# Performance work log

Hardware: AMD Instinct MI355X
Metric: run time of the kernel (lower is better)

The kernel has to match this reference:

```python
import jax, jax.numpy as jnp
import numpy as np

N_NODES = 50000


def setup_inputs() -> dict:
    key = jax.random.key(0)
    k_x, k_e, k_w1, k_w2 = jax.random.split(key, 4)
    in_c, hid, out_c = 256, 128, 64
    x = jax.random.normal(k_x, (N_NODES, in_c), dtype=jnp.float32)
    edge_index = jax.random.randint(k_e, (2, 800000), 0, N_NODES, dtype=jnp.int64)
    # Glorot-ish scaled weights (faithful to GCNConv default init scale)
    W1 = jax.random.normal(k_w1, (in_c, hid), dtype=jnp.float32) * (1.0 / np.sqrt(in_c))
    b1 = jnp.zeros((hid,), dtype=jnp.float32)
    W2 = jax.random.normal(k_w2, (hid, out_c), dtype=jnp.float32) * (1.0 / np.sqrt(hid))
    b2 = jnp.zeros((out_c,), dtype=jnp.float32)
    return {"x": x, "edge_index": edge_index, "W1": W1, "b1": b1, "W2": W2, "b2": b2}


def _gcn_norm(edge_index, n_nodes):
    # Add self loops, compute symmetric normalization D^-1/2 A D^-1/2.
    loop = jnp.arange(n_nodes, dtype=edge_index.dtype)
    src = jnp.concatenate([edge_index[0], loop])
    dst = jnp.concatenate([edge_index[1], loop])
    deg = jax.ops.segment_sum(jnp.ones_like(dst, dtype=jnp.float32), dst,
                              num_segments=n_nodes)
    dis = jnp.where(deg > 0, jax.lax.rsqrt(deg), 0.0)  # deg_inv_sqrt
    norm = dis[src] * dis[dst]  # [E + N]
    return src, dst, norm


def _gcn_conv(x, W, b, src, dst, norm, n_nodes):
    h = x @ W                                  # [N, F_out] dense transform first
    msgs = h[src] * norm[:, None]              # edge-wise gather + scale
    agg = jax.ops.segment_sum(msgs, dst, num_segments=n_nodes)  # scatter-add
    return agg + b


def reference(x, edge_index, W1, b1, W2, b2):
    n = x.shape[0]
    src, dst, norm = _gcn_norm(edge_index, n)  # cached=True: same norm both layers
    h = _gcn_conv(x, W1, b1, src, dst, norm, n)
    h = jax.nn.relu(h)
    # Dropout is identity in eval mode (deterministic reference)
    return _gcn_conv(h, W2, b2, src, dst, norm, n)
```

## Files before the change

kernel.cpp:

```cpp
#include <hip/hip_runtime.h>


#define IN_C 256
#define HID 128
#define OUTC 64
#define NBLK 128

typedef __attribute__((ext_vector_type(8))) short short8;
typedef __attribute__((ext_vector_type(4))) float f32x4;

__device__ __forceinline__ void gload_lds16(const void* src, void* dst) {
    __builtin_amdgcn_global_load_lds(
        (const __attribute__((address_space(1))) unsigned int*)src,
        (__attribute__((address_space(3))) unsigned int*)dst, 16, 0, 0);
}

__device__ __forceinline__ void bf16split(float f, ushort& h, ushort& l) {
    unsigned u = __float_as_uint(f);
    h = (ushort)(u >> 16);
    float hf = __uint_as_float(u & 0xFFFF0000u);
    unsigned v = __float_as_uint(f - hf);
    l = (ushort)((v + 0x7FFF + ((v >> 16) & 1)) >> 16);
}

__device__ __forceinline__ void cvt8(float4 f0, float4 f1, short8& hi8, short8& lo8) {
    float ff[8];
    *(float4*)&ff[0] = f0; *(float4*)&ff[4] = f1;
    unsigned* hp = (unsigned*)&hi8;
    unsigned* lp = (unsigned*)&lo8;
    #pragma unroll
    for (int i = 0; i < 4; ++i) {
        unsigned u0 = __float_as_uint(ff[2 * i]), u1 = __float_as_uint(ff[2 * i + 1]);
        unsigned hf0 = u0 & 0xFFFF0000u, hf1 = u1 & 0xFFFF0000u;
        hp[i] = (u0 >> 16) | hf1;
        float r0 = ff[2 * i]     - __uint_as_float(hf0);
        float r1 = ff[2 * i + 1] - __uint_as_float(hf1);
        lp[i] = (__float_as_uint(r0) >> 16) | (__float_as_uint(r1) & 0xFFFF0000u);
    }
}

__device__ __forceinline__ ushort f2bf(float f) {
    unsigned u = __float_as_uint(f);
    return (ushort)((u + 0x7FFF + ((u >> 16) & 1)) >> 16);
}
__device__ __forceinline__ float bf2f(ushort u) {
    return __uint_as_float((unsigned)u << 16);
}

__device__ __forceinline__ int edge_at(const void* ei, long long idx, int is32) {
    return is32 ? ((const int*)ei)[idx] : (int)((const long long*)ei)[idx];
}

__global__ void detect_kernel(const unsigned long long* ei, int* flag) {
    if (threadIdx.x == 0 && blockIdx.x == 0) {
        int is32 = 0;
        for (int i = 0; i < 64; ++i)
            if (ei[i] >> 32) { is32 = 1; break; }
        *flag = is32;
    }
}

__global__ __launch_bounds__(256) void wtrans_kernel(const float* __restrict__ W1,
                                                     const float* __restrict__ W2,
                                                     ushort* __restrict__ wf1,
                                                     ushort* __restrict__ wf2) {
    int id = blockIdx.x * 256 + threadIdx.x;
    if (id < 8192) {
        int lane = id & 63, r = id >> 6;
        int pl = r & 1, nt = (r >> 1) & 7, kidx = r >> 4;
        int n = nt * 16 + (lane & 15);
        int kb = kidx * 32 + (lane >> 4) * 8;
        ushort v[8];
        #pragma unroll
        for (int j = 0; j < 8; ++j) {
            ushort h, l; bf16split(W1[(kb + j) * HID + n], h, l);
            v[j] = pl ? l : h;
        }
        *(short8*)&wf1[(size_t)id * 8] = *(short8*)v;
    } else if (id < 10240) {
        int id2 = id - 8192;
        int lane = id2 & 63, r = id2 >> 6;
        int pl = r & 1, nt = (r >> 1) & 3, kidx = r >> 3;
        int n = nt * 16 + (lane & 15);
        int kb = kidx * 32 + (lane >> 4) * 8;
        ushort v[8];
        #pragma unroll
        for (int j = 0; j < 8; ++j) {
            ushort h, l; bf16split(W2[(kb + j) * OUTC + n], h, l);
            v[j] = pl ? l : h;
        }
        *(short8*)&wf2[(size_t)id2 * 8] = *(short8*)v;
    }
}

__global__ __launch_bounds__(256) void bin_count(const void* ei, const int* __restrict__ flag,
                                                 int* __restrict__ blkcnt, int E, int nb) {
    __shared__ int h[256];
    int t = threadIdx.x;
    h[t] = 0;
    __syncthreads();
    int is32 = *flag;
    int chunk = (E + gridDim.x - 1) / gridDim.x;
    long long s0 = (long long)blockIdx.x * chunk;
    long long s1 = s0 + chunk; if (s1 > E) s1 = E;
    for (long long e = s0 + t; e < s1; e += 256) {
        int d = edge_at(ei, (long long)E + e, is32);
        atomicAdd(&h[d >> 8], 1);
    }
    __syncthreads();
    if (t < nb) blkcnt[t * NBLK + blockIdx.x] = h[t];
}

__global__ __launch_bounds__(256) void bin_scan(int* __restrict__ blkcnt,
                                                int* __restrict__ bbase, int nb) {
    __shared__ int sh[256];
    int t = threadIdx.x;
    int tot = 0;
    if (t < nb) {
        int4* p = (int4*)&blkcnt[t * NBLK];
        int run = 0;
        for (int i = 0; i < NBLK / 4; ++i) {
            int4 v = p[i]; int4 o;
            o.x = run; run += v.x; o.y = run; run += v.y;
            o.z = run; run += v.z; o.w = run; run += v.w;
            p[i] = o;
        }
        tot = run;
    }
    sh[t] = tot;
    __syncthreads();
    for (int d = 1; d < 256; d <<= 1) {
        int add = (t >= d) ? sh[t - d] : 0;
        __syncthreads();
        sh[t] += add;
        __syncthreads();
    }
    if (t < nb) {
        bbase[t] = sh[t] - tot;
        if (t == nb - 1) bbase[nb] = sh[t];
    }
}

__global__ __launch_bounds__(256) void bin_scatter(const void* ei, const int* __restrict__ flag,
                                                   const int* __restrict__ blkcnt,
                                                   const int* __restrict__ bbase,
                                                   unsigned* __restrict__ coarse, int E, int nb) {
    __shared__ int cur[256];
    int t = threadIdx.x;
    if (t < nb) cur[t] = bbase[t] + blkcnt[t * NBLK + blockIdx.x];
    __syncthreads();
    int is32 = *flag;
    int chunk = (E + gridDim.x - 1) / gridDim.x;
    long long s0 = (long long)blockIdx.x * chunk;
    long long s1 = s0 + chunk; if (s1 > E) s1 = E;
    for (long long e = s0 + t; e < s1; e += 256) {
        int s = edge_at(ei, e, is32);
        int d = edge_at(ei, (long long)E + e, is32);
        int p = atomicAdd(&cur[d >> 8], 1);
        coarse[p] = (unsigned)s | ((unsigned)(d & 255) << 17);
    }
}

__global__ __launch_bounds__(256) void fine_kernel(const unsigned* __restrict__ coarse,
                                                   const int* __restrict__ bbase,
                                                   int* __restrict__ row_ptr,
                                                   float* __restrict__ dis,
                                                   int* __restrict__ epk, int N, int nb) {
    __shared__ int h[256], cur[256], sh[256];
    int b = blockIdx.x, t = threadIdx.x;
    int nb0 = b << 8;
    int e0b = bbase[b], e1b = bbase[b + 1];
    h[t] = 0;
    __syncthreads();
    for (int e = e0b + t; e < e1b; e += 256)
        atomicAdd(&h[(coarse[e] >> 17) & 0xFF], 1);
    __syncthreads();
    int cnt = h[t];
    sh[t] = cnt;
    __syncthreads();
    for (int d = 1; d < 256; d <<= 1) {
        int add = (t >= d) ? sh[t - d] : 0;
        __syncthreads();
        sh[t] += add;
        __syncthreads();
    }
    int excl = sh[t] - cnt;
    int node = nb0 + t;
    if (node < N) {
        row_ptr[node] = e0b + excl;
        dis[node] = rsqrtf((float)cnt + 1.0f);
        if (node == N - 1) row_ptr[N] = e0b + sh[t];
    }
    cur[t] = e0b + excl;
    __syncthreads();
    for (int e = e0b + t; e < e1b; e += 256) {
        unsigned r = coarse[e];
        int p = atomicAdd(&cur[(r >> 17) & 0xFF], 1);
        epk[p] = (int)(r & 0x1FFFF);
    }
}

__global__ void zsent_kernel(ushort* a, ushort* b, ushort* c) {
    int t = threadIdx.x;
    if (t < 64) { a[t] = 0; b[t] = 0; c[t] = 0; }
}

__global__ __launch_bounds__(256) void gemm1_mfma(const float* __restrict__ X,
                                                  const ushort* __restrict__ wf1,
                                                  const float* __restrict__ dis,
                                                  ushort* __restrict__ HB, int N) {
    __shared__ float xs[64 * 64];
    int t = threadIdx.x;
    int lane = t & 63, w = t >> 6;
    int m_off = (w >> 1) * 32, n_off = (w & 1) * 64;
    long long row0 = (long long)blockIdx.x * 64;
    size_t sstride = (size_t)(N + 1) * 64;
    f32x4 acc[2][4] = {};
    for (int k0i = 0; k0i < 4; ++k0i) {
        __syncthreads();
        #pragma unroll
        for (int i = 0; i < 4; ++i) {
            int lrow = w * 16 + i * 4 + (lane >> 4);
            long long gr = row0 + lrow; if (gr >= N) gr = N - 1;
            int gchunk = (lane & 15) ^ (lrow & 7);
            gload_lds16(X + gr * IN_C + k0i * 64 + gchunk * 4,
                        xs + (w * 16 + i * 4) * 64);
        }
        __syncthreads();
        #pragma unroll
        for (int kk = 0; kk < 2; ++kk) {
            int kidx = k0i * 2 + kk;
            short8 ah[2], al[2], bh[4], bl[4];
            #pragma unroll
            for (int ni = 0; ni < 4; ++ni) {
                int nt = (n_off >> 4) + ni;
                const ushort* bp = wf1 + (size_t)(kidx * 16 + nt * 2) * 512 + lane * 8;
                bh[ni] = *(const short8*)bp;
                bl[ni] = *(const short8*)(bp + 512);
            }
            #pragma unroll
            for (int mi = 0; mi < 2; ++mi) {
                int r = m_off + mi * 16 + (lane & 15);
                int s = r & 7;
                int c0 = kk * 8 + (lane >> 4) * 2;
                float4 f0 = *(float4*)((char*)xs + r * 256 + ((c0 ^ s) * 16));
                float4 f1 = *(float4*)((char*)xs + r * 256 + (((c0 + 1) ^ s) * 16));
                cvt8(f0, f1, ah[mi], al[mi]);
            }
            #pragma unroll
            for (int mi = 0; mi < 2; ++mi)
                #pragma unroll
                for (int ni = 0; ni < 4; ++ni) {
                    acc[mi][ni] = __builtin_amdgcn_mfma_f32_16x16x32_bf16(ah[mi], bh[ni], acc[mi][ni], 0, 0, 0);
                    acc[mi][ni] = __builtin_amdgcn_mfma_f32_16x16x32_bf16(ah[mi], bl[ni], acc[mi][ni], 0, 0, 0);
                    acc[mi][ni] = __builtin_amdgcn_mfma_f32_16x16x32_bf16(al[mi], bh[ni], acc[mi][ni], 0, 0, 0);
                }
        }
    }
    int cr = (lane >> 4) * 4, cc = lane & 15;
    #pragma unroll
    for (int mi = 0; mi < 2; ++mi)
        #pragma unroll
        for (int j = 0; j < 4; ++j) {
            long long gr = row0 + m_off + mi * 16 + cr + j;
            if (gr < N) {
                float dv = dis[gr];
                #pragma unroll
                for (int ni = 0; ni < 4; ++ni) {
                    int col = n_off + ni * 16 + cc;
                    HB[(size_t)(col >> 6) * sstride + gr * 64 + (col & 63)] =
                        f2bf(acc[mi][ni][j] * dv);
                }
            }
        }
}

__global__ __launch_bounds__(256) void gemm2_mfma(const ushort* __restrict__ Ah,
                                                  const ushort* __restrict__ Al,
                                                  const ushort* __restrict__ wf2,
                                                  const float* __restrict__ dis,
                                                  ushort* __restrict__ HB, int N) {
    __shared__ ushort ash[64 * 64], asl[64 * 64];
    int t = threadIdx.x;
    int lane = t & 63, w = t >> 6;
    int m_off = (w >> 1) * 32, n_off = (w & 1) * 32;
    long long row0 = (long long)blockIdx.x * 64;
    f32x4 acc[2][2] = {};
    for (int k0i = 0; k0i < 2; ++k0i) {
        __syncthreads();
        #pragma unroll
        for (int i = 0; i < 2; ++i) {
            int rbase = w * 16 + i * 8;
            long long gr = row0 + rbase + (lane >> 3);
            size_t so = (size_t)gr * 128 + k0i * 64 + (lane & 7) * 8;
            gload_lds16(Ah + so, ash + rbase * 64);
            gload_lds16(Al + so, asl + rbase * 64);
        }
        __syncthreads();
        #pragma unroll
        for (int kk = 0; kk < 2; ++kk) {
            int kidx = k0i * 2 + kk;
            short8 ah[2], al[2], bh[2], bl[2];
            #pragma unroll
            for (int ni = 0; ni < 2; ++ni) {
                int nt = (n_off >> 4) + ni;
                const ushort* bp = wf2 + (size_t)(kidx * 8 + nt * 2) * 512 + lane * 8;
                bh[ni] = *(const short8*)bp;
                bl[ni] = *(const short8*)(bp + 512);
            }
            #pragma unroll
            for (int mi = 0; mi < 2; ++mi) {
                int r = m_off + mi * 16 + (lane & 15);
                int pos = (kk * 4 + (lane >> 4)) ^ (r & 7);
                ah[mi] = *(short8*)((char*)ash + r * 128 + pos * 16);
                al[mi] = *(short8*)((char*)asl + r * 128 + pos * 16);
            }
            #pragma unroll
            for (int mi = 0; mi < 2; ++mi)
                #pragma unroll
                for (int ni = 0; ni < 2; ++ni) {
                    acc[mi][ni] = __builtin_amdgcn_mfma_f32_16x16x32_bf16(ah[mi], bh[ni], acc[mi][ni], 0, 0, 0);
                    acc[mi][ni] = __builtin_amdgcn_mfma_f32_16x16x32_bf16(ah[mi], bl[ni], acc[mi][ni], 0, 0, 0);
                    acc[mi][ni] = __builtin_amdgcn_mfma_f32_16x16x32_bf16(al[mi], bh[ni], acc[mi][ni], 0, 0, 0);
                }
        }
    }
    int cr = (lane >> 4) * 4, cc = lane & 15;
    #pragma unroll
    for (int mi = 0; mi < 2; ++mi)
        #pragma unroll
        for (int j = 0; j < 4; ++j) {
            long long gr = row0 + m_off + mi * 16 + cr + j;
            if (gr < N) {
                float dv = dis[gr];
                #pragma unroll
                for (int ni = 0; ni < 2; ++ni)
                    HB[gr * OUTC + n_off + ni * 16 + cc] = f2bf(acc[mi][ni][j] * dv);
            }
        }
}

template <int MODE>
__global__ __launch_bounds__(256) void seg_agg_v6(const ushort* __restrict__ Hsl,
                                                  const float* __restrict__ dis,
                                                  const int* __restrict__ row_ptr,
                                                  const int* __restrict__ epk,
                                                  const float* __restrict__ bias,
                                                  float* __restrict__ outF,
                                                  ushort* __restrict__ outH,
                                                  ushort* __restrict__ outL,
                                                  int N, int sl) {
    int lane = threadIdx.x & 63;
    int node = (int)(((long long)blockIdx.x * blockDim.x + threadIdx.x) >> 6);
    if (node >= N) return;
    const ushort* hl = Hsl + lane;
    float acc = bf2f(hl[node * 64]);
    int e0 = row_ptr[node], e1 = row_ptr[node + 1];
    for (int base = e0; base < e1; base += 64) {
        int cnt = min(64, e1 - base);
        int rec = epk[min(base + lane, e1 - 1)];
        for (int u0 = 0; u0 < cnt; u0 += 16) {
            float hv[16];
            #pragma unroll
            for (int u = 0; u < 16; ++u) {
                int s = (u0 + u < cnt) ? __builtin_amdgcn_readlane(rec, u0 + u) : N;
                hv[u] = bf2f(hl[s * 64]);
            }
            #pragma unroll
            for (int u = 0; u < 16; ++u)
                acc += hv[u];
        }
    }
    float r = dis[node] * acc;
    if constexpr (MODE == 0) {
        float a2 = fmaxf(r + bias[sl * 64 + lane], 0.f);
        unsigned u = __float_as_uint(a2);
        ushort h = (ushort)(u >> 16);
        float rr = a2 - __uint_as_float(u & 0xFFFF0000u);
        ushort l = (ushort)(__float_as_uint(rr) >> 16);
        int col = sl * 64 + ((((lane >> 3) ^ (node & 7))) << 3) + (lane & 7);
        outH[(size_t)node * 128 + col] = h;
        outL[(size_t)node * 128 + col] = l;
    } else {
        outF[(size_t)node * 64 + lane] = r + bias[lane];
    }
}

extern "C" void kernel_launch(void* const* d_in, const int* in_sizes, int n_in,
                              void* d_out, int out_size, void* d_ws, size_t ws_size,
                              hipStream_t stream) {
    const float* x  = (const float*)d_in[0];
    const void*  ei = d_in[1];
    const float* W1 = (const float*)d_in[2];
    const float* b1 = (const float*)d_in[3];
    const float* W2 = (const float*)d_in[4];
    const float* b2 = (const float*)d_in[5];
    float* out = (float*)d_out;
    int N = in_sizes[0] / IN_C;
    int E = in_sizes[1] / 2;
    int nb = (N + 255) >> 8;
    int nblk64 = (N + 63) / 64;
    int N_pad = nblk64 * 64;

    char* ws = (char*)d_ws;
    size_t off = 0;
    auto alloc = [&](size_t bytes) {
        void* p = ws + off;
        off += ((bytes + 255) / 256) * 256;
        return p;
    };
    int*      flag    = (int*)alloc(4);
    int*      blkcnt  = (int*)alloc((size_t)nb * NBLK * 4);
    int*      bbase   = (int*)alloc(((size_t)nb + 1) * 4);
    int*      row_ptr = (int*)alloc(((size_t)N + 1) * 4);
    float*    dis     = (float*)alloc((size_t)N * 4);
    unsigned* coarse  = (unsigned*)alloc((size_t)E * 4);
    int*      epk     = (int*)alloc((size_t)E * 4);
    ushort*   wf1     = (ushort*)alloc(131072);
    ushort*   wf2     = (ushort*)alloc(32768);
    size_t sstride    = (size_t)(N + 1) * 64;
    ushort*   H1b     = (ushort*)alloc(2 * sstride * 2);
    ushort*   Ah      = (ushort*)alloc((size_t)N_pad * 128 * 2);
    ushort*   Al      = (ushort*)alloc((size_t)N_pad * 128 * 2);
    ushort*   H2b     = (ushort*)alloc(sstride * 2);

    detect_kernel<<<1, 64, 0, stream>>>((const unsigned long long*)ei, flag);
    wtrans_kernel<<<40, 256, 0, stream>>>(W1, W2, wf1, wf2);
    bin_count<<<NBLK, 256, 0, stream>>>(ei, flag, blkcnt, E, nb);
    bin_scan<<<1, 256, 0, stream>>>(blkcnt, bbase, nb);
    bin_scatter<<<NBLK, 256, 0, stream>>>(ei, flag, blkcnt, bbase, coarse, E, nb);
    fine_kernel<<<nb, 256, 0, stream>>>(coarse, bbase, row_ptr, dis, epk, N, nb);
    zsent_kernel<<<1, 64, 0, stream>>>(H1b + (size_t)N * 64,
                                       H1b + sstride + (size_t)N * 64,
                                       H2b + (size_t)N * 64);
    gemm1_mfma<<<nblk64, 256, 0, stream>>>(x, wf1, dis, H1b, N);

    int agg_blocks = (int)(((long long)N * 64 + 255) / 256);
    seg_agg_v6<0><<<agg_blocks, 256, 0, stream>>>(H1b,           dis, row_ptr, epk,
                                                  b1, nullptr, Ah, Al, N, 0);
    seg_agg_v6<0><<<agg_blocks, 256, 0, stream>>>(H1b + sstride, dis, row_ptr, epk,
                                                  b1, nullptr, Ah, Al, N, 1);
    gemm2_mfma<<<nblk64, 256, 0, stream>>>(Ah, Al, wf2, dis, H2b, N);
    seg_agg_v6<1><<<agg_blocks, 256, 0, stream>>>(H2b, dis, row_ptr, epk,
                                                  b2, out, nullptr, nullptr, N, 0);
}
```

Measured before the change: 160.2 us.

## Merge layer-1 aggregation launches, sort neighbors by source half, widen binning grid

Raises the number of binning blocks from 128 to 512 so the edge count and scatter pass is spread over more CUs. Within each destination node's neighbour list, the fine sort now groups sources into a lower and an upper half of the node range, which aims to improve gather locality in the L2/MALL. The two layer-1 aggregation launches are merged into one launch that covers both feature slices, removing a launch and its tail. The extra half-key doubles the LDS histogram and adds a compare per edge, and the per-block binning counts grow with the larger grid.

```diff
diff --git a/kernel.cpp b/kernel.cpp
--- a/kernel.cpp
+++ b/kernel.cpp
@@ -4,7 +4,7 @@
 #define IN_C 256
 #define HID 128
 #define OUTC 64
-#define NBLK 128
+#define NBLK 512
 
 typedef __attribute__((ext_vector_type(8))) short short8;
 typedef __attribute__((ext_vector_type(4))) float f32x4;
@@ -165,37 +165,44 @@
                                                    const int* __restrict__ bbase,
                                                    int* __restrict__ row_ptr,
                                                    float* __restrict__ dis,
-                                                   int* __restrict__ epk, int N, int nb) {
-    __shared__ int h[256], cur[256], sh[256];
+                                                   int* __restrict__ epk,
+                                                   int N, int nb, int half) {
+    __shared__ int h[512], cur[512], ssum[256];
     int b = blockIdx.x, t = threadIdx.x;
     int nb0 = b << 8;
     int e0b = bbase[b], e1b = bbase[b + 1];
-    h[t] = 0;
-    __syncthreads();
-    for (int e = e0b + t; e < e1b; e += 256)
-        atomicAdd(&h[(coarse[e] >> 17) & 0xFF], 1);
-    __syncthreads();
-    int cnt = h[t];
-    sh[t] = cnt;
+    h[t] = 0; h[t + 256] = 0;
+    __syncthreads();
+    for (int e = e0b + t; e < e1b; e += 256) {
+        unsigned r = coarse[e];
+        int key = (((r >> 17) & 0xFF) << 1) | ((int)(r & 0x1FFFF) >= half ? 1 : 0);
+        atomicAdd(&h[key], 1);
+    }
+    __syncthreads();
+    int v0 = h[2 * t], v1 = h[2 * t + 1];
+    int s = v0 + v1;
+    ssum[t] = s;
     __syncthreads();
     for (int d = 1; d < 256; d <<= 1) {
-        int add = (t >= d) ? sh[t - d] : 0;
-        __syncthreads();
-        sh[t] += add;
-        __syncthreads();
-    }
-    int excl = sh[t] - cnt;
+        int add = (t >= d) ? ssum[t - d] : 0;
+        __syncthreads();
+        ssum[t] += add;
+        __syncthreads();
+    }
+    int excl = ssum[t] - s;
     int node = nb0 + t;
     if (node < N) {
         row_ptr[node] = e0b + excl;
-        dis[node] = rsqrtf((float)cnt + 1.0f);
-        if (node == N - 1) row_ptr[N] = e0b + sh[t];
-    }
-    cur[t] = e0b + excl;
+        dis[node] = rsqrtf((float)s + 1.0f);
+        if (node == N - 1) row_ptr[N] = e0b + ssum[t];
+    }
+    cur[2 * t] = e0b + excl;
+    cur[2 * t + 1] = e0b + excl + v0;
     __syncthreads();
     for (int e = e0b + t; e < e1b; e += 256) {
         unsigned r = coarse[e];
-        int p = atomicAdd(&cur[(r >> 17) & 0xFF], 1);
+        int key = (((r >> 17) & 0xFF) << 1) | ((int)(r & 0x1FFFF) >= half ? 1 : 0);
+        int p = atomicAdd(&cur[key], 1);
         epk[p] = (int)(r & 0x1FFFF);
     }
 }
@@ -341,7 +348,7 @@
 }
 
 template <int MODE>
-__global__ __launch_bounds__(256) void seg_agg_v6(const ushort* __restrict__ Hsl,
+__global__ __launch_bounds__(256) void seg_agg_v7(const ushort* __restrict__ Hbase,
                                                   const float* __restrict__ dis,
                                                   const int* __restrict__ row_ptr,
                                                   const int* __restrict__ epk,
@@ -349,11 +356,16 @@
                                                   float* __restrict__ outF,
                                                   ushort* __restrict__ outH,
                                                   ushort* __restrict__ outL,
-                                                  int N, int sl) {
+                                                  int N, size_t sstride) {
     int lane = threadIdx.x & 63;
-    int node = (int)(((long long)blockIdx.x * blockDim.x + threadIdx.x) >> 6);
+    long long gw = ((long long)blockIdx.x * blockDim.x + threadIdx.x) >> 6;
+    int sl = 0;
+    int node = (int)gw;
+    if constexpr (MODE == 0) {
+        if (node >= N) { sl = 1; node -= N; }
+    }
     if (node >= N) return;
-    const ushort* hl = Hsl + lane;
+    const ushort* hl = Hbase + (size_t)sl * sstride + lane;
     float acc = bf2f(hl[node * 64]);
     int e0 = row_ptr[node], e1 = row_ptr[node + 1];
     for (int base = e0; base < e1; base += 64) {
@@ -429,18 +441,17 @@
     bin_count<<<NBLK, 256, 0, stream>>>(ei, flag, blkcnt, E, nb);
     bin_scan<<<1, 256, 0, stream>>>(blkcnt, bbase, nb);
     bin_scatter<<<NBLK, 256, 0, stream>>>(ei, flag, blkcnt, bbase, coarse, E, nb);
-    fine_kernel<<<nb, 256, 0, stream>>>(coarse, bbase, row_ptr, dis, epk, N, nb);
+    fine_kernel<<<nb, 256, 0, stream>>>(coarse, bbase, row_ptr, dis, epk, N, nb, N / 2);
     zsent_kernel<<<1, 64, 0, stream>>>(H1b + (size_t)N * 64,
                                        H1b + sstride + (size_t)N * 64,
                                        H2b + (size_t)N * 64);
     gemm1_mfma<<<nblk64, 256, 0, stream>>>(x, wf1, dis, H1b, N);
 
-    int agg_blocks = (int)(((long long)N * 64 + 255) / 256);
-    seg_agg_v6<0><<<agg_blocks, 256, 0, stream>>>(H1b,           dis, row_ptr, epk,
-                                                  b1, nullptr, Ah, Al, N, 0);
-    seg_agg_v6<0><<<agg_blocks, 256, 0, stream>>>(H1b + sstride, dis, row_ptr, epk,
-                                                  b1, nullptr, Ah, Al, N, 1);
+    int agg1_blocks = (int)(((long long)N * 2 * 64 + 255) / 256);
+    int agg2_blocks = (int)(((long long)N * 64 + 255) / 256);
+    seg_agg_v7<0><<<agg1_blocks, 256, 0, stream>>>(H1b, dis, row_ptr, epk,
+                                                   b1, nullptr, Ah, Al, N, sstride);
     gemm2_mfma<<<nblk64, 256, 0, stream>>>(Ah, Al, wf2, dis, H2b, N);
-    seg_agg_v6<1><<<agg_blocks, 256, 0, stream>>>(H2b, dis, row_ptr, epk,
-                                                  b2, out, nullptr, nullptr, N, 0);
-}
+    seg_agg_v7<1><<<agg2_blocks, 256, 0, stream>>>(H2b, dis, row_ptr, epk,
+                                                   b2, out, nullptr, nullptr, N, sstride);
+}
```

After: 170.8 us. 1.07x slower.

## Store layer-1 features row-contiguous and aggregate both halves in one pass

Applied to the files above, without the earlier changes.

The GEMM1 output changes from two 64-column slabs to a single row-major [N+1,128] bf16 layout. The layer-1 aggregation now runs as one kernel in which each lane loads a 32-bit pair of bf16 values per neighbor, replacing two launches that each gathered 64 columns. This halves the index loads and the readlane/loop overhead per edge and doubles the bytes per gather transaction. In exchange, each wave keeps two accumulators, and the 256-byte row gathers may change cache-line behaviour.

```diff
diff --git a/kernel.cpp b/kernel.cpp
--- a/kernel.cpp
+++ b/kernel.cpp
@@ -200,9 +200,10 @@
     }
 }
 
-__global__ void zsent_kernel(ushort* a, ushort* b, ushort* c) {
-    int t = threadIdx.x;
-    if (t < 64) { a[t] = 0; b[t] = 0; c[t] = 0; }
+__global__ void zsent_kernel(ushort* h1, ushort* h2) {
+    int t = threadIdx.x;
+    if (t < 128) h1[t] = 0;
+    if (t < 64)  h2[t] = 0;
 }
 
 __global__ __launch_bounds__(256) void gemm1_mfma(const float* __restrict__ X,
@@ -214,7 +215,6 @@
     int lane = t & 63, w = t >> 6;
     int m_off = (w >> 1) * 32, n_off = (w & 1) * 64;
     long long row0 = (long long)blockIdx.x * 64;
-    size_t sstride = (size_t)(N + 1) * 64;
     f32x4 acc[2][4] = {};
     for (int k0i = 0; k0i < 4; ++k0i) {
         __syncthreads();
@@ -268,8 +268,7 @@
                 #pragma unroll
                 for (int ni = 0; ni < 4; ++ni) {
                     int col = n_off + ni * 16 + cc;
-                    HB[(size_t)(col >> 6) * sstride + gr * 64 + (col & 63)] =
-                        f2bf(acc[mi][ni][j] * dv);
+                    HB[gr * HID + col] = f2bf(acc[mi][ni][j] * dv);
                 }
             }
         }
@@ -341,7 +340,7 @@
 }
 
 template <int MODE>
-__global__ __launch_bounds__(256) void seg_agg_v6(const ushort* __restrict__ Hsl,
+__global__ __launch_bounds__(256) void seg_agg_v8(const ushort* __restrict__ H,
                                                   const float* __restrict__ dis,
                                                   const int* __restrict__ row_ptr,
                                                   const int* __restrict__ epk,
@@ -349,40 +348,66 @@
                                                   float* __restrict__ outF,
                                                   ushort* __restrict__ outH,
                                                   ushort* __restrict__ outL,
-                                                  int N, int sl) {
+                                                  int N) {
     int lane = threadIdx.x & 63;
     int node = (int)(((long long)blockIdx.x * blockDim.x + threadIdx.x) >> 6);
     if (node >= N) return;
-    const ushort* hl = Hsl + lane;
-    float acc = bf2f(hl[node * 64]);
     int e0 = row_ptr[node], e1 = row_ptr[node + 1];
-    for (int base = e0; base < e1; base += 64) {
-        int cnt = min(64, e1 - base);
-        int rec = epk[min(base + lane, e1 - 1)];
-        for (int u0 = 0; u0 < cnt; u0 += 16) {
-            float hv[16];
-            #pragma unroll
-            for (int u = 0; u < 16; ++u) {
-                int s = (u0 + u < cnt) ? __builtin_amdgcn_readlane(rec, u0 + u) : N;
-                hv[u] = bf2f(hl[s * 64]);
-            }
-            #pragma unroll
-            for (int u = 0; u < 16; ++u)
-                acc += hv[u];
-        }
-    }
-    float r = dis[node] * acc;
     if constexpr (MODE == 0) {
-        float a2 = fmaxf(r + bias[sl * 64 + lane], 0.f);
-        unsigned u = __float_as_uint(a2);
-        ushort h = (ushort)(u >> 16);
-        float rr = a2 - __uint_as_float(u & 0xFFFF0000u);
-        ushort l = (ushort)(__float_as_uint(rr) >> 16);
-        int col = sl * 64 + ((((lane >> 3) ^ (node & 7))) << 3) + (lane & 7);
-        outH[(size_t)node * 128 + col] = h;
-        outL[(size_t)node * 128 + col] = l;
+        const unsigned* hl = (const unsigned*)H + lane;
+        unsigned v = hl[node * 64];
+        float a0 = bf2f((ushort)v), a1 = bf2f((ushort)(v >> 16));
+        for (int base = e0; base < e1; base += 64) {
+            int cnt = min(64, e1 - base);
+            int rec = epk[min(base + lane, e1 - 1)];
+            for (int u0 = 0; u0 < cnt; u0 += 16) {
+                unsigned hv[16];
+                #pragma unroll
+                for (int u = 0; u < 16; ++u) {
+                    int s = (u0 + u < cnt) ? __builtin_amdgcn_readlane(rec, u0 + u) : N;
+                    hv[u] = hl[s * 64];
+                }
+                #pragma unroll
+                for (int u = 0; u < 16; ++u) {
+                    a0 += bf2f((ushort)hv[u]);
+                    a1 += bf2f((ushort)(hv[u] >> 16));
+                }
+            }
+        }
+        float dn = dis[node];
+        int c0 = lane * 2;
+        float2 bb = *(const float2*)&bias[c0];
+        float p0 = fmaxf(dn * a0 + bb.x, 0.f);
+        float p1 = fmaxf(dn * a1 + bb.y, 0.f);
+        unsigned u0b = __float_as_uint(p0), u1b = __float_as_uint(p1);
+        unsigned h0 = u0b >> 16, h1 = u1b >> 16;
+        float r0 = p0 - __uint_as_float(u0b & 0xFFFF0000u);
+        float r1 = p1 - __uint_as_float(u1b & 0xFFFF0000u);
+        unsigned l0 = __float_as_uint(r0) >> 16, l1 = __float_as_uint(r1) >> 16;
+        int sl = c0 >> 6, e = c0 & 63;
+        int ch = ((e >> 3) ^ (node & 7));
+        size_t pos = (size_t)node * 128 + sl * 64 + ch * 8 + (e & 7);
+        *(unsigned*)&outH[pos] = h0 | (h1 << 16);
+        *(unsigned*)&outL[pos] = l0 | (l1 << 16);
     } else {
-        outF[(size_t)node * 64 + lane] = r + bias[lane];
+        const ushort* hl = H + lane;
+        float acc = bf2f(hl[node * 64]);
+        for (int base = e0; base < e1; base += 64) {
+            int cnt = min(64, e1 - base);
+            int rec = epk[min(base + lane, e1 - 1)];
+            for (int u0 = 0; u0 < cnt; u0 += 16) {
+                float hv[16];
+                #pragma unroll
+                for (int u = 0; u < 16; ++u) {
+                    int s = (u0 + u < cnt) ? __builtin_amdgcn_readlane(rec, u0 + u) : N;
+                    hv[u] = bf2f(hl[s * 64]);
+                }
+                #pragma unroll
+                for (int u = 0; u < 16; ++u)
+                    acc += hv[u];
+            }
+        }
+        outF[(size_t)node * 64 + lane] = dis[node] * acc + bias[lane];
     }
 }
 
@@ -418,11 +443,10 @@
     int*      epk     = (int*)alloc((size_t)E * 4);
     ushort*   wf1     = (ushort*)alloc(131072);
     ushort*   wf2     = (ushort*)alloc(32768);
-    size_t sstride    = (size_t)(N + 1) * 64;
-    ushort*   H1b     = (ushort*)alloc(2 * sstride * 2);
+    ushort*   H1b     = (ushort*)alloc(((size_t)N + 1) * HID * 2);
     ushort*   Ah      = (ushort*)alloc((size_t)N_pad * 128 * 2);
     ushort*   Al      = (ushort*)alloc((size_t)N_pad * 128 * 2);
-    ushort*   H2b     = (ushort*)alloc(sstride * 2);
+    ushort*   H2b     = (ushort*)alloc(((size_t)N + 1) * OUTC * 2);
 
     detect_kernel<<<1, 64, 0, stream>>>((const unsigned long long*)ei, flag);
     wtrans_kernel<<<40, 256, 0, stream>>>(W1, W2, wf1, wf2);
@@ -430,17 +454,13 @@
     bin_scan<<<1, 256, 0, stream>>>(blkcnt, bbase, nb);
     bin_scatter<<<NBLK, 256, 0, stream>>>(ei, flag, blkcnt, bbase, coarse, E, nb);
     fine_kernel<<<nb, 256, 0, stream>>>(coarse, bbase, row_ptr, dis, epk, N, nb);
-    zsent_kernel<<<1, 64, 0, stream>>>(H1b + (size_t)N * 64,
-                                       H1b + sstride + (size_t)N * 64,
-                                       H2b + (size_t)N * 64);
+    zsent_kernel<<<1, 128, 0, stream>>>(H1b + (size_t)N * HID, H2b + (size_t)N * OUTC);
     gemm1_mfma<<<nblk64, 256, 0, stream>>>(x, wf1, dis, H1b, N);
 
     int agg_blocks = (int)(((long long)N * 64 + 255) / 256);
-    seg_agg_v6<0><<<agg_blocks, 256, 0, stream>>>(H1b,           dis, row_ptr, epk,
-                                                  b1, nullptr, Ah, Al, N, 0);
-    seg_agg_v6<0><<<agg_blocks, 256, 0, stream>>>(H1b + sstride, dis, row_ptr, epk,
-                                                  b1, nullptr, Ah, Al, N, 1);
+    seg_agg_v8<0><<<agg_blocks, 256, 0, stream>>>(H1b, dis, row_ptr, epk,
+                                                  b1, nullptr, Ah, Al, N);
     gemm2_mfma<<<nblk64, 256, 0, stream>>>(Ah, Al, wf2, dis, H2b, N);
-    seg_agg_v6<1><<<agg_blocks, 256, 0, stream>>>(H2b, dis, row_ptr, epk,
-                                                  b2, out, nullptr, nullptr, N, 0);
-}
+    seg_agg_v8<1><<<agg_blocks, 256, 0, stream>>>(H2b, dis, row_ptr, epk,
+                                                  b2, out, nullptr, nullptr, N);
+}
```

Result: faster. 142.1 us (-11.3%).
